# Performance work log

Hardware: AMD Instinct MI355X
Metric: run time of the kernel (lower is better)

Reference implementation:

```python
import jax, jax.numpy as jnp
import numpy as np

B, T, D = 16, 1024, 1024
H, HS = 16, 64  # num_heads, attention_head_size; H*HS == D
NEG_INF = -1e9


def setup_inputs() -> dict:
    key = jax.random.key(0)
    ks = jax.random.split(key, 6)
    s = 0.02
    x = jax.random.normal(ks[0], (B, T, D), dtype=jnp.float32)
    Wq = jax.random.normal(ks[1], (D, HS), dtype=jnp.float32) * s
    Wk = jax.random.normal(ks[2], (D, HS), dtype=jnp.float32) * s
    Wv = jax.random.normal(ks[3], (D, HS), dtype=jnp.float32) * s
    Wp = jax.random.normal(ks[4], (D, D), dtype=jnp.float32) * s
    bp = jax.random.normal(ks[5], (D,), dtype=jnp.float32) * s
    return {"x": x, "Wq": Wq, "Wk": Wk, "Wv": Wv, "Wp": Wp, "bp": bp}


def reference(x, Wq, Wk, Wv, Wp, bp):
    # Single shared Head (ModuleList([Head(...)] * num_heads) shares weights).
    q = jnp.einsum('btd,dh->bth', x, Wq)  # [B,T,HS]
    k = jnp.einsum('btd,dh->bth', x, Wk)
    v = jnp.einsum('btd,dh->bth', x, Wv)
    scale = 1.0 / jnp.sqrt(jnp.float32(HS))
    scores = jnp.einsum('bth,bsh->bts', q, k) * scale  # [B,T,T]
    causal = jnp.tril(jnp.ones((T, T), dtype=bool))
    scores = jnp.where(causal[None, :, :], scores, NEG_INF)
    attn = jax.nn.softmax(scores, axis=-1)
    head_out = jnp.einsum('bts,bsh->bth', attn, v)  # [B,T,HS]
    # Concatenate H identical head outputs along feature dim -> [B,T,D]
    out = jnp.tile(head_out, (1, 1, H))
    out = jnp.einsum('btd,de->bte', out, Wp) + bp
    return out
```

## Files before the change

kernel.cpp:

```cpp
#include <hip/hip_runtime.h>
#include <hip/hip_bf16.h>
#include <cstddef>

typedef __attribute__((ext_vector_type(8))) __bf16 bf16x8;
typedef __attribute__((ext_vector_type(4))) float f32x4;
typedef unsigned long long ull_t;

static __device__ __forceinline__ unsigned short f2bf(float f) {
    __bf16 h = (__bf16)f;
    return __builtin_bit_cast(unsigned short, h);
}

__global__ void prep_weights(const float* __restrict__ Wq, const float* __restrict__ Wk,
                             const float* __restrict__ Wv, const float* __restrict__ Wp,
                             unsigned short* __restrict__ Wfrag,
                             unsigned short* __restrict__ WpFrag) {
    int blk = blockIdx.x;
    if (blk < 768) {
        int idx = blk * 256 + threadIdx.x;
        int CB = idx >> 14;
        int rem = idx & 16383;
        int S = rem >> 9;
        int r2 = rem & 511;
        int l = r2 >> 3, j = r2 & 7;
        int col = CB * 16 + (l & 15);
        int k = S * 32 + (l >> 4) * 8 + j;
        float v;
        if (col < 64)       v = Wq[k * 64 + col];
        else if (col < 128) v = Wk[k * 64 + (col - 64)];
        else                v = Wv[k * 64 + (col - 128)];
        Wfrag[idx] = f2bf(v);
    } else {
        int idx = (blk - 768) * 256 + threadIdx.x;
        int CB = idx >> 10;
        int rem = idx & 1023;
        int s = rem >> 9;
        int r2 = rem & 511;
        int l = r2 >> 3, j = r2 & 7;
        int col = CB * 16 + (l & 15);
        int h = s * 32 + (l >> 4) * 8 + j;
        float sum = 0.f;
#pragma unroll
        for (int j16 = 0; j16 < 16; ++j16) sum += Wp[(size_t)(j16 * 64 + h) * 1024 + col];
        WpFrag[idx] = f2bf(sum);
    }
}

__global__ __launch_bounds__(256) void qkv_gemm(const float* __restrict__ x,
                                                const unsigned short* __restrict__ Wfrag,
                                                unsigned short* __restrict__ qs,
                                                unsigned short* __restrict__ ks,
                                                unsigned short* __restrict__ vT) {
    __shared__ __align__(16) unsigned short xl[2][32 * 128];

    const int tid = threadIdx.x;
    const int lane = tid & 63;
    const int w = tid >> 6;
    const int g = lane >> 4, c = lane & 15;
    const int row0 = blockIdx.x * 32;

    const int srow = tid >> 3;
    const int scolf = (tid & 7) * 16;
    const float* xsrc = x + (size_t)(row0 + srow) * 1024 + scolf;
    const int sdst0 = srow * 256 + ((scolf * 2) ^ ((srow & 7) << 4));
    const int sdst1 = srow * 256 + ((scolf * 2 + 16) ^ ((srow & 7) << 4));

    const unsigned short* wbase = Wfrag + (size_t)(w * 3) * 32 * 512 + lane * 8;

    f32x4 acc[2][3];
#pragma unroll
    for (int mr = 0; mr < 2; ++mr)
#pragma unroll
        for (int cb = 0; cb < 3; ++cb) acc[mr][cb] = (f32x4){0.f, 0.f, 0.f, 0.f};

    float4 pre0[4], pre1[4];
#pragma unroll
    for (int i = 0; i < 4; ++i) pre0[i] = *(const float4*)(xsrc + i * 4);
#pragma unroll
    for (int i = 0; i < 4; ++i) pre1[i] = *(const float4*)(xsrc + 128 + i * 4);

    bf16x8 bP[3][6];
#pragma unroll
    for (int pp = 0; pp < 2; ++pp) {
#pragma unroll
        for (int i = 0; i < 6; ++i) {
            int SB = pp * 2 + (i / 3);
            int cb = i % 3;
            bP[pp][i] = *(const bf16x8*)(wbase + ((size_t)(cb * 32 + SB) * 512));
        }
    }

    {
        bf16x8 v0, v1;
#pragma unroll
        for (int j = 0; j < 4; ++j) { v0[j] = (__bf16)pre0[0][j]; v0[4 + j] = (__bf16)pre0[1][j]; }
#pragma unroll
        for (int j = 0; j < 4; ++j) { v1[j] = (__bf16)pre0[2][j]; v1[4 + j] = (__bf16)pre0[3][j]; }
        *(bf16x8*)((char*)xl[0] + sdst0) = v0;
        *(bf16x8*)((char*)xl[0] + sdst1) = v1;
    }
    __syncthreads();

#pragma unroll
    for (int p = 0; p < 16; ++p) {
        const int t = p >> 1;
        if ((p & 1) == 0 && t + 2 < 8) {
            if ((t & 1) == 0) {
#pragma unroll
                for (int i = 0; i < 4; ++i) pre0[i] = *(const float4*)(xsrc + (t + 2) * 128 + i * 4);
            } else {
#pragma unroll
                for (int i = 0; i < 4; ++i) pre1[i] = *(const float4*)(xsrc + (t + 2) * 128 + i * 4);
            }
        }
        if (p + 2 < 16) {
#pragma unroll
            for (int i = 0; i < 6; ++i) {
                int SB = (p + 2) * 2 + (i / 3);
                int cb = i % 3;
                bP[(p + 2) % 3][i] = *(const bf16x8*)(wbase + ((size_t)(cb * 32 + SB) * 512));
            }
        }
#pragma unroll
        for (int sl = 0; sl < 2; ++sl) {
            int s = (p & 1) * 2 + sl;
            bf16x8 af[2];
#pragma unroll
            for (int mr = 0; mr < 2; ++mr)
                af[mr] = *(const bf16x8*)((char*)xl[t & 1] + (mr * 16 + c) * 256 +
                                          ((s * 64 + g * 16) ^ ((c & 7) << 4)));
#pragma unroll
            for (int cb = 0; cb < 3; ++cb) {
                acc[0][cb] = __builtin_amdgcn_mfma_f32_16x16x32_bf16(af[0], bP[p % 3][sl * 3 + cb], acc[0][cb], 0, 0, 0);
                acc[1][cb] = __builtin_amdgcn_mfma_f32_16x16x32_bf16(af[1], bP[p % 3][sl * 3 + cb], acc[1][cb], 0, 0, 0);
            }
        }
        if (p & 1) {
            if (t < 7) {
                bf16x8 v0, v1;
                if ((t & 1) == 0) {
#pragma unroll
                    for (int j = 0; j < 4; ++j) { v0[j] = (__bf16)pre1[0][j]; v0[4 + j] = (__bf16)pre1[1][j]; }
#pragma unroll
                    for (int j = 0; j < 4; ++j) { v1[j] = (__bf16)pre1[2][j]; v1[4 + j] = (__bf16)pre1[3][j]; }
                    *(bf16x8*)((char*)xl[1] + sdst0) = v0;
                    *(bf16x8*)((char*)xl[1] + sdst1) = v1;
                } else {
#pragma unroll
                    for (int j = 0; j < 4; ++j) { v0[j] = (__bf16)pre0[0][j]; v0[4 + j] = (__bf16)pre0[1][j]; }
#pragma unroll
                    for (int j = 0; j < 4; ++j) { v1[j] = (__bf16)pre0[2][j]; v1[4 + j] = (__bf16)pre0[3][j]; }
                    *(bf16x8*)((char*)xl[0] + sdst0) = v0;
                    *(bf16x8*)((char*)xl[0] + sdst1) = v1;
                }
            }
            __syncthreads();
        }
    }

    const float QSCALE = 0.125f * 1.44269504088896340736f;
#pragma unroll
    for (int mr = 0; mr < 2; ++mr) {
#pragma unroll
        for (int cb = 0; cb < 3; ++cb) {
            int col = w * 48 + cb * 16 + c;
            int rowb = row0 + mr * 16 + g * 4;
            if (col < 64) {
#pragma unroll
                for (int r = 0; r < 4; ++r)
                    qs[(size_t)(rowb + r) * 64 + col] = f2bf(acc[mr][cb][r] * QSCALE);
            } else if (col < 128) {
#pragma unroll
                for (int r = 0; r < 4; ++r)
                    ks[(size_t)(rowb + r) * 64 + (col - 64)] = f2bf(acc[mr][cb][r]);
            } else {
                int h = col - 128;
                int bb = rowb >> 10, trow = rowb & 1023;
                ull_t dv =
                    (ull_t)f2bf(acc[mr][cb][0]) |
                    ((ull_t)f2bf(acc[mr][cb][1]) << 16) |
                    ((ull_t)f2bf(acc[mr][cb][2]) << 32) |
                    ((ull_t)f2bf(acc[mr][cb][3]) << 48);
                *(ull_t*)(vT + (size_t)bb * 65536 + (size_t)h * 1024 + trow) = dv;
            }
        }
    }
}

__global__ __launch_bounds__(256) void attn_proj(const unsigned short* __restrict__ qs,
                                                 const unsigned short* __restrict__ ks,
                                                 const unsigned short* __restrict__ vT,
                                                 const unsigned short* __restrict__ WpFrag,
                                                 const float* __restrict__ bp,
                                                 float* __restrict__ out) {
    __shared__ unsigned short Plds[4][16 * 40];
    __shared__ float oL[2][1024];
    __shared__ float pL[2][256];
    __shared__ __align__(16) unsigned short hl[2][16 * 64];

    const int tid = threadIdx.x;
    const int lane = tid & 63;
    const int wid = tid >> 6;
    const int tslot = wid >> 1;
    const int half = wid & 1;
    const int g = lane >> 4, c = lane & 15;

    const int xcd = blockIdx.x & 7;
    const int k8 = blockIdx.x >> 3;
    const int bb = 2 * xcd + tslot;
    const int qidx = 63 - k8;
    const int qr0 = qidx * 16;
    const int qend = qr0 + 16;
    const int nc = (qidx >> 1) + 1;
    const int c0 = half ? (nc >> 1) : 0;
    const int c1 = half ? nc : (nc >> 1);

    const unsigned short* qbase = qs + ((size_t)bb * 1024 + qr0 + c) * 64 + g * 8;
    bf16x8 aq0 = *(const bf16x8*)(qbase);
    bf16x8 aq1 = *(const bf16x8*)(qbase + 32);

    const unsigned short* kB = ks + (size_t)bb * 1024 * 64;
    const unsigned short* vB = vT + (size_t)bb * 64 * 1024;

    f32x4 o[4];
#pragma unroll
    for (int i = 0; i < 4; ++i) o[i] = (f32x4){0.f, 0.f, 0.f, 0.f};
    float psum[4] = {0.f, 0.f, 0.f, 0.f};
    const f32x4 zero = {0.f, 0.f, 0.f, 0.f};

    bf16x8 kc0, kc1, kc2, kc3, vc0, vc1, vc2, vc3;
    if (c0 < c1) {
        const unsigned short* kp = kB + (size_t)(c0 * 32 + c) * 64 + g * 8;
        kc0 = *(const bf16x8*)(kp);
        kc1 = *(const bf16x8*)(kp + 32);
        kc2 = *(const bf16x8*)(kp + 16 * 64);
        kc3 = *(const bf16x8*)(kp + 16 * 64 + 32);
        const unsigned short* vp = vB + (size_t)c * 1024 + c0 * 32 + g * 8;
        vc0 = *(const bf16x8*)(vp);
        vc1 = *(const bf16x8*)(vp + 16 * 1024);
        vc2 = *(const bf16x8*)(vp + 32 * 1024);
        vc3 = *(const bf16x8*)(vp + 48 * 1024);
    }

    for (int ci = c0; ci < c1; ++ci) {
        const int j0 = ci * 32;
        const bool full = (j0 + 16 < qend);
        f32x4 s0 = __builtin_amdgcn_mfma_f32_16x16x32_bf16(aq0, kc0, zero, 0, 0, 0);
        s0 = __builtin_amdgcn_mfma_f32_16x16x32_bf16(aq1, kc1, s0, 0, 0, 0);
        f32x4 s1 = zero;
        if (full) {
            s1 = __builtin_amdgcn_mfma_f32_16x16x32_bf16(aq0, kc2, zero, 0, 0, 0);
            s1 = __builtin_amdgcn_mfma_f32_16x16x32_bf16(aq1, kc3, s1, 0, 0, 0);
        }

        bf16x8 kn0, kn1, kn2, kn3, vn0, vn1, vn2, vn3;
        if (ci + 1 < c1) {
            const int jn = (ci + 1) * 32;
            const unsigned short* kp = kB + (size_t)(jn + c) * 64 + g * 8;
            kn0 = *(const bf16x8*)(kp);
            kn1 = *(const bf16x8*)(kp + 32);
            kn2 = *(const bf16x8*)(kp + 16 * 64);
            kn3 = *(const bf16x8*)(kp + 16 * 64 + 32);
            const unsigned short* vp = vB + (size_t)c * 1024 + jn + g * 8;
            vn0 = *(const bf16x8*)(vp);
            vn1 = *(const bf16x8*)(vp + 16 * 1024);
            vn2 = *(const bf16x8*)(vp + 32 * 1024);
            vn3 = *(const bf16x8*)(vp + 48 * 1024);
        }

#pragma unroll
        for (int r = 0; r < 4; ++r) {
            int t = qr0 + g * 4 + r;
            float e0 = (j0 + c > t) ? 0.f : exp2f(s0[r]);
            float e1 = (!full || j0 + 16 + c > t) ? 0.f : exp2f(s1[r]);
            psum[r] += e0 + e1;
            Plds[wid][(g * 4 + r) * 40 + c]      = f2bf(e0);
            Plds[wid][(g * 4 + r) * 40 + 16 + c] = f2bf(e1);
        }
        bf16x8 pa = *(const bf16x8*)(&Plds[wid][c * 40 + g * 8]);
        o[0] = __builtin_amdgcn_mfma_f32_16x16x32_bf16(pa, vc0, o[0], 0, 0, 0);
        o[1] = __builtin_amdgcn_mfma_f32_16x16x32_bf16(pa, vc1, o[1], 0, 0, 0);
        o[2] = __builtin_amdgcn_mfma_f32_16x16x32_bf16(pa, vc2, o[2], 0, 0, 0);
        o[3] = __builtin_amdgcn_mfma_f32_16x16x32_bf16(pa, vc3, o[3], 0, 0, 0);

        kc0 = kn0; kc1 = kn1; kc2 = kn2; kc3 = kn3;
        vc0 = vn0; vc1 = vn1; vc2 = vn2; vc3 = vn3;
    }

    if (half == 1) {
#pragma unroll
        for (int hb = 0; hb < 4; ++hb)
            *(f32x4*)&oL[tslot][(hb * 64 + lane) * 4] = o[hb];
        f32x4 pv = {psum[0], psum[1], psum[2], psum[3]};
        *(f32x4*)&pL[tslot][lane * 4] = pv;
    }
    __syncthreads();
    if (half == 0) {
        f32x4 pv = *(const f32x4*)&pL[tslot][lane * 4];
        float inv[4];
#pragma unroll
        for (int r = 0; r < 4; ++r) {
            float ps = psum[r] + pv[r];
            ps += __shfl_xor(ps, 1);
            ps += __shfl_xor(ps, 2);
            ps += __shfl_xor(ps, 4);
            ps += __shfl_xor(ps, 8);
            inv[r] = 1.f / ps;
        }
#pragma unroll
        for (int hb = 0; hb < 4; ++hb) {
            f32x4 po = *(const f32x4*)&oL[tslot][(hb * 64 + lane) * 4];
#pragma unroll
            for (int r = 0; r < 4; ++r) {
                int row = g * 4 + r;
                int colb = (hb * 16 + c) * 2;
                *(unsigned short*)((char*)hl[tslot] + row * 128 + (colb ^ ((row & 7) << 4))) =
                    f2bf((o[hb][r] + po[r]) * inv[r]);
            }
        }
    }
    __syncthreads();

    bf16x8 a0t0 = *(const bf16x8*)((char*)hl[0] + c * 128 + ((g * 16) ^ ((c & 7) << 4)));
    bf16x8 a1t0 = *(const bf16x8*)((char*)hl[0] + c * 128 + ((64 + g * 16) ^ ((c & 7) << 4)));
    bf16x8 a0t1 = *(const bf16x8*)((char*)hl[1] + c * 128 + ((g * 16) ^ ((c & 7) << 4)));
    bf16x8 a1t1 = *(const bf16x8*)((char*)hl[1] + c * 128 + ((64 + g * 16) ^ ((c & 7) << 4)));
    const int b0 = 2 * xcd;
    const int b1 = 2 * xcd + 1;
    const size_t obase0 = ((size_t)b0 * 1024 + qr0) * 1024;
    const size_t obase1 = ((size_t)b1 * 1024 + qr0) * 1024;
#pragma unroll
    for (int cb = 0; cb < 16; ++cb) {
        int CB = wid * 16 + cb;
        bf16x8 wb0 = *(const bf16x8*)(WpFrag + (size_t)(CB * 2 + 0) * 512 + lane * 8);
        bf16x8 wb1 = *(const bf16x8*)(WpFrag + (size_t)(CB * 2 + 1) * 512 + lane * 8);
        f32x4 acc0 = __builtin_amdgcn_mfma_f32_16x16x32_bf16(a0t0, wb0, zero, 0, 0, 0);
        acc0 = __builtin_amdgcn_mfma_f32_16x16x32_bf16(a1t0, wb1, acc0, 0, 0, 0);
        f32x4 acc1 = __builtin_amdgcn_mfma_f32_16x16x32_bf16(a0t1, wb0, zero, 0, 0, 0);
        acc1 = __builtin_amdgcn_mfma_f32_16x16x32_bf16(a1t1, wb1, acc1, 0, 0, 0);
        int col = CB * 16 + c;
        float bias = bp[col];
#pragma unroll
        for (int r = 0; r < 4; ++r) {
            out[obase0 + (size_t)(g * 4 + r) * 1024 + col] = acc0[r] + bias;
            out[obase1 + (size_t)(g * 4 + r) * 1024 + col] = acc1[r] + bias;
        }
    }
}

extern "C" void kernel_launch(void* const* d_in, const int* in_sizes, int n_in,
                              void* d_out, int out_size, void* d_ws, size_t ws_size,
                              hipStream_t stream) {
    (void)in_sizes; (void)n_in; (void)out_size; (void)ws_size;
    const float* x  = (const float*)d_in[0];
    const float* Wq = (const float*)d_in[1];
    const float* Wk = (const float*)d_in[2];
    const float* Wv = (const float*)d_in[3];
    const float* Wp = (const float*)d_in[4];
    const float* bp = (const float*)d_in[5];
    float* out = (float*)d_out;

    const size_t NTOK = 16 * 1024;
    unsigned short* ws = (unsigned short*)d_ws;
    unsigned short* qs     = ws;
    unsigned short* ks     = qs + NTOK * 64;
    unsigned short* vT     = ks + NTOK * 64;
    unsigned short* Wfrag  = vT + NTOK * 64;
    unsigned short* WpFrag = Wfrag + 192 * 1024;

    prep_weights<<<1024, 256, 0, stream>>>(Wq, Wk, Wv, Wp, Wfrag, WpFrag);
    qkv_gemm<<<512, 256, 0, stream>>>(x, Wfrag, qs, ks, vT);
    attn_proj<<<512, 256, 0, stream>>>(qs, ks, vT, WpFrag, bp, out);
}
```

Before: 56.89 us.

## Move Wp head-sum into qkv_gemm extra blocks and vectorize Wqkv prep

Result: slower. 59.88 us (+5.3%).

```diff
diff --git a/kernel.cpp b/kernel.cpp
--- a/kernel.cpp
+++ b/kernel.cpp
@@ -11,46 +11,56 @@
     return __builtin_bit_cast(unsigned short, h);
 }
 
-__global__ void prep_weights(const float* __restrict__ Wq, const float* __restrict__ Wk,
-                             const float* __restrict__ Wv, const float* __restrict__ Wp,
-                             unsigned short* __restrict__ Wfrag,
-                             unsigned short* __restrict__ WpFrag) {
-    int blk = blockIdx.x;
-    if (blk < 768) {
-        int idx = blk * 256 + threadIdx.x;
-        int CB = idx >> 14;
-        int rem = idx & 16383;
-        int S = rem >> 9;
-        int r2 = rem & 511;
-        int l = r2 >> 3, j = r2 & 7;
-        int col = CB * 16 + (l & 15);
-        int k = S * 32 + (l >> 4) * 8 + j;
-        float v;
-        if (col < 64)       v = Wq[k * 64 + col];
-        else if (col < 128) v = Wk[k * 64 + (col - 64)];
-        else                v = Wv[k * 64 + (col - 128)];
-        Wfrag[idx] = f2bf(v);
-    } else {
-        int idx = (blk - 768) * 256 + threadIdx.x;
-        int CB = idx >> 10;
-        int rem = idx & 1023;
-        int s = rem >> 9;
-        int r2 = rem & 511;
-        int l = r2 >> 3, j = r2 & 7;
-        int col = CB * 16 + (l & 15);
-        int h = s * 32 + (l >> 4) * 8 + j;
-        float sum = 0.f;
-#pragma unroll
-        for (int j16 = 0; j16 < 16; ++j16) sum += Wp[(size_t)(j16 * 64 + h) * 1024 + col];
-        WpFrag[idx] = f2bf(sum);
-    }
+__global__ void prep_wqkv(const float* __restrict__ Wq, const float* __restrict__ Wk,
+                          const float* __restrict__ Wv, unsigned short* __restrict__ Wfrag) {
+    int gid = blockIdx.x * 256 + threadIdx.x;
+    int m = gid >> 13;
+    int rem = gid & 8191;
+    int khi = rem >> 6;
+    int lcol = rem & 63;
+    const float* W = (m == 0) ? Wq : (m == 1) ? Wk : Wv;
+    bf16x8 v;
+#pragma unroll
+    for (int j = 0; j < 8; ++j)
+        v[j] = (__bf16)W[(khi * 8 + j) * 64 + lcol];
+    int CB = m * 4 + (lcol >> 4);
+    int S = khi >> 2;
+    int lane = ((khi & 3) << 4) | (lcol & 15);
+    *(bf16x8*)(Wfrag + ((size_t)(CB * 32 + S) * 512 + lane * 8)) = v;
 }
 
 __global__ __launch_bounds__(256) void qkv_gemm(const float* __restrict__ x,
                                                 const unsigned short* __restrict__ Wfrag,
                                                 unsigned short* __restrict__ qs,
                                                 unsigned short* __restrict__ ks,
-                                                unsigned short* __restrict__ vT) {
+                                                unsigned short* __restrict__ vT,
+                                                const float* __restrict__ Wp,
+                                                unsigned short* __restrict__ WpFrag) {
+    if (blockIdx.x >= 512) {
+        int gid = (blockIdx.x - 512) * 256 + threadIdx.x;
+        int h = gid >> 7;
+        int cc = gid & 127;
+        float s0 = 0.f, s1 = 0.f, s2 = 0.f, s3 = 0.f, s4 = 0.f, s5 = 0.f, s6 = 0.f, s7 = 0.f;
+#pragma unroll
+        for (int j16 = 0; j16 < 16; ++j16) {
+            const float* row = Wp + (size_t)(j16 * 64 + h) * 1024 + cc * 8;
+            float4 a = *(const float4*)(row);
+            float4 b = *(const float4*)(row + 4);
+            s0 += a.x; s1 += a.y; s2 += a.z; s3 += a.w;
+            s4 += b.x; s5 += b.y; s6 += b.z; s7 += b.w;
+        }
+        float sum[8] = {s0, s1, s2, s3, s4, s5, s6, s7};
+        int sp = h >> 5, hi = (h >> 3) & 3, j = h & 7;
+#pragma unroll
+        for (int q = 0; q < 8; ++q) {
+            int col = cc * 8 + q;
+            int lane = (hi << 4) | (col & 15);
+            int CB = col >> 4;
+            WpFrag[(size_t)(CB * 2 + sp) * 512 + lane * 8 + j] = f2bf(sum[q]);
+        }
+        return;
+    }
+
     __shared__ __align__(16) unsigned short xl[2][32 * 128];
 
     const int tid = threadIdx.x;
@@ -368,7 +378,7 @@
     unsigned short* Wfrag  = vT + NTOK * 64;
     unsigned short* WpFrag = Wfrag + 192 * 1024;
 
-    prep_weights<<<1024, 256, 0, stream>>>(Wq, Wk, Wv, Wp, Wfrag, WpFrag);
-    qkv_gemm<<<512, 256, 0, stream>>>(x, Wfrag, qs, ks, vT);
+    prep_wqkv<<<96, 256, 0, stream>>>(Wq, Wk, Wv, Wfrag);
+    qkv_gemm<<<544, 256, 0, stream>>>(x, Wfrag, qs, ks, vT, Wp, WpFrag);
     attn_proj<<<512, 256, 0, stream>>>(qs, ks, vT, WpFrag, bp, out);
 }
```
